# Optimization experiments

Hardware: AMD Instinct MI355X
Metric: run time of the kernel (lower is better)

The kernel has to match this reference:

```python
import jax, jax.numpy as jnp
import numpy as np

N_NODES = 500_000
D_IN = 256
D_ATT = 128
NUM_GRAPHS = 4096


def setup_inputs() -> dict:
    key = jax.random.key(0)
    k_x, k_b, k_w1, k_b1, k_w2, k_b2 = jax.random.split(key, 6)
    x = jax.random.normal(k_x, (N_NODES, D_IN), dtype=jnp.float32)
    batch = jnp.sort(jax.random.randint(k_b, (N_NODES,), 0, NUM_GRAPHS, dtype=jnp.int64))
    # attention_net params: Linear(D_IN, D_ATT) -> tanh -> Linear(D_ATT, 1)
    s1 = 1.0 / np.sqrt(D_IN)
    s2 = 1.0 / np.sqrt(D_ATT)
    W1 = jax.random.uniform(k_w1, (D_IN, D_ATT), minval=-s1, maxval=s1, dtype=jnp.float32)
    b1 = jax.random.uniform(k_b1, (D_ATT,), minval=-s1, maxval=s1, dtype=jnp.float32)
    W2 = jax.random.uniform(k_w2, (D_ATT, 1), minval=-s2, maxval=s2, dtype=jnp.float32)
    b2 = jax.random.uniform(k_b2, (1,), minval=-s2, maxval=s2, dtype=jnp.float32)
    return {"x": x, "batch": batch, "num_graphs": NUM_GRAPHS,
            "W1": W1, "b1": b1, "W2": W2, "b2": b2}


def reference(x, batch, num_graphs, W1, b1, W2, b2):
    # attention_weights = Linear -> tanh -> Linear  (dropout is identity in eval)
    h = jnp.tanh(x @ W1 + b1)              # [N, D_ATT]
    attn = h @ W2 + b2                      # [N, 1]
    weighted_x = x * attn                   # [N, D_IN]
    # global_add_pool: segment-sum over graph ids
    return jax.ops.segment_sum(weighted_x, batch, num_segments=num_graphs)  # [B, D_IN]
```

## Files before the change

### kernel.cpp

```cpp
#include <hip/hip_runtime.h>
#include <hip/hip_bf16.h>

#define NN     500000
#define DIN    256
#define DATT   128
#define NG     4096
#define MT     32
#define NT32   15625
#define NBLOCKS 768
#define TPB    21

typedef __attribute__((ext_vector_type(8))) short short8;
typedef __attribute__((ext_vector_type(4))) float f32x4;

__device__ __forceinline__ unsigned int pack2bf(float a, float b) {
    unsigned int ua = __float_as_uint(a) + 0x8000u;
    unsigned int ub = __float_as_uint(b) + 0x8000u;
    return __builtin_amdgcn_perm(ub, ua, 0x07060302);
}

__device__ __forceinline__ float tanh_fast(float v) {
    float e = __expf(2.f * v);
    return 1.f - 2.f * __builtin_amdgcn_rcpf(e + 1.f);
}

__device__ __forceinline__ void lds_barrier() {
    asm volatile("s_waitcnt lgkmcnt(0)" ::: "memory");
    __builtin_amdgcn_s_barrier();
    asm volatile("" ::: "memory");
}

__global__ void prep_w1t(const float* __restrict__ W1, unsigned short* __restrict__ W1t) {
    int c = blockIdx.x;
    int k = threadIdx.x;
    unsigned int u = __float_as_uint(W1[k * DATT + c]) + 0x8000u;
    W1t[c * DIN + k] = (unsigned short)(u >> 16);
}

__global__ __launch_bounds__(256, 3)
void attnpool_kernel(const float* __restrict__ x,
                     const int* __restrict__ batch,
                     const unsigned short* __restrict__ W1t,
                     const float* __restrict__ b1,
                     const float* __restrict__ W2,
                     const float* __restrict__ b2,
                     float* __restrict__ out)
{
    __shared__ unsigned short xb[2][MT * DIN];
    __shared__ float part[4][MT];

    const int t0 = blockIdx.x * TPB;
    if (t0 >= NT32) return;
    const int tEnd = (t0 + TPB < NT32) ? t0 + TPB : NT32;

    const int tid = threadIdx.x;
    const int w   = tid >> 6;
    const int l   = tid & 63;
    const int lr  = l & 15;
    const int lg  = l >> 4;

    short8 afr[16];
    {
        const unsigned short* A0 = W1t + (32 * w + lr) * DIN;
        #pragma unroll
        for (int kc = 0; kc < 8; ++kc) {
            afr[kc]     = *reinterpret_cast<const short8*>(A0 + 32 * kc + 8 * lg);
            afr[8 + kc] = *reinterpret_cast<const short8*>(A0 + 16 * DIN + 32 * kc + 8 * lg);
        }
    }
    float4 b1v[2], w2v[2];
    #pragma unroll
    for (int r2 = 0; r2 < 2; ++r2) {
        int c0 = 32 * w + 16 * r2 + 4 * lg;
        b1v[r2] = *reinterpret_cast<const float4*>(&b1[c0]);
        w2v[r2] = *reinterpret_cast<const float4*>(&W2[c0]);
    }
    const float b2s = b2[0];

    const float4* xg = (const float4*)x;
    float4 pf[8];
    {
        int base = t0 * (MT * 64);
        #pragma unroll
        for (int i = 0; i < 8; ++i) pf[i] = xg[base + tid + i * 256];
    }

    float accum = 0.f;
    int gcur = -1;
    int cur = 0;

    for (int t = t0; t < tEnd; ++t) {
        unsigned short* X = xb[cur];
        #pragma unroll
        for (int i = 0; i < 8; ++i) {
            int j = tid + i * 256;
            int r = j >> 6, c4 = j & 63;
            int byte = r * 512 + ((c4 * 8) ^ ((r & 7) << 4));
            *reinterpret_cast<uint2*>(reinterpret_cast<char*>(X) + byte) =
                make_uint2(pack2bf(pf[i].x, pf[i].y), pack2bf(pf[i].z, pf[i].w));
        }
        int bvt = -1;
        if (l < 32) {
            int g = batch[t * MT + l];
            bvt = ((unsigned)g < NG) ? g : -1;
        }
        lds_barrier();

        if (t + 1 < tEnd) {
            int base = (t + 1) * (MT * 64);
            #pragma unroll
            for (int i = 0; i < 8; ++i) pf[i] = xg[base + tid + i * 256];
        }

        f32x4 acc[2][2];
        #pragma unroll
        for (int r2 = 0; r2 < 2; ++r2)
            #pragma unroll
            for (int ct = 0; ct < 2; ++ct)
                acc[r2][ct] = (f32x4){0.f, 0.f, 0.f, 0.f};

        #pragma unroll
        for (int kc = 0; kc < 8; ++kc) {
            int ko = 32 * kc + 8 * lg;
            short8 bfr[2];
            #pragma unroll
            for (int ct = 0; ct < 2; ++ct) {
                int row = 16 * ct + lr;
                int byte = row * 512 + ((ko * 2) ^ ((row & 7) << 4));
                bfr[ct] = *reinterpret_cast<const short8*>(reinterpret_cast<const char*>(X) + byte);
            }
            #pragma unroll
            for (int ct = 0; ct < 2; ++ct) {
                acc[0][ct] = __builtin_amdgcn_mfma_f32_16x16x32_bf16(afr[kc],     bfr[ct], acc[0][ct], 0, 0, 0);
                acc[1][ct] = __builtin_amdgcn_mfma_f32_16x16x32_bf16(afr[8 + kc], bfr[ct], acc[1][ct], 0, 0, 0);
            }
        }

        #pragma unroll
        for (int ct = 0; ct < 2; ++ct) {
            float p = 0.f;
            #pragma unroll
            for (int r2 = 0; r2 < 2; ++r2) {
                p += tanh_fast(acc[r2][ct][0] + b1v[r2].x) * w2v[r2].x;
                p += tanh_fast(acc[r2][ct][1] + b1v[r2].y) * w2v[r2].y;
                p += tanh_fast(acc[r2][ct][2] + b1v[r2].z) * w2v[r2].z;
                p += tanh_fast(acc[r2][ct][3] + b1v[r2].w) * w2v[r2].w;
            }
            p += __shfl_xor(p, 16, 64);
            p += __shfl_xor(p, 32, 64);
            if (lg == 0) part[w][16 * ct + lr] = p;
        }
        lds_barrier();

        const int nd = l & 31;
        float va = b2s + part[0][nd] + part[1][nd] + part[2][nd] + part[3][nd];

        #pragma unroll
        for (int n = 0; n < MT; ++n) {
            int   g = __builtin_amdgcn_readlane(bvt, n);
            float a = __int_as_float(__builtin_amdgcn_readlane(__float_as_int(va), n));
            if (g != gcur) {
                if (gcur >= 0) atomicAdd(&out[gcur * DIN + tid], accum);
                accum = 0.f;
                gcur = g;
            }
            int byte = n * 512 + ((tid * 2) ^ ((n & 7) << 4));
            float xv = __uint_as_float(
                (unsigned int)(*reinterpret_cast<const unsigned short*>(
                    reinterpret_cast<const char*>(X) + byte)) << 16);
            accum = fmaf(a, xv, accum);
        }
        cur ^= 1;
    }
    if (gcur >= 0) atomicAdd(&out[gcur * DIN + tid], accum);
}

extern "C" void kernel_launch(void* const* d_in, const int* in_sizes, int n_in,
                              void* d_out, int out_size, void* d_ws, size_t ws_size,
                              hipStream_t stream) {
    const float* x     = (const float*)d_in[0];
    const int*   batch = (const int*)d_in[1];
    const float* W1 = (const float*)d_in[3];
    const float* b1 = (const float*)d_in[4];
    const float* W2 = (const float*)d_in[5];
    const float* b2 = (const float*)d_in[6];
    float* out = (float*)d_out;
    unsigned short* W1t = (unsigned short*)d_ws;

    hipMemsetAsync(out, 0, (size_t)NG * DIN * sizeof(float), stream);
    prep_w1t<<<DATT, DIN, 0, stream>>>(W1, W1t);
    attnpool_kernel<<<NBLOCKS, 256, 0, stream>>>(x, batch, W1t, b1, W2, b2, out);
}
```

Baseline: 156.7 us.

## Double block size to 512 threads, splitting MFMA columns and pooling across waves

Moves to 512-thread blocks with 8 waves. Each wave now computes 16 of the attention columns instead of 32, and the pooling loop is split so each half of the block handles 16 of the 32 nodes per tile. The grid shrinks from 768 to 512 blocks, each covering more tiles. The goal is to cut per-wave register pressure and serial pooling work and to raise occupancy. The cost is more LDS partial sums, more barrier participants and more atomics, since both halves flush separately.

```diff
diff --git a/kernel.cpp b/kernel.cpp
--- a/kernel.cpp
+++ b/kernel.cpp
@@ -7,8 +7,8 @@
 #define NG     4096
 #define MT     32
 #define NT32   15625
-#define NBLOCKS 768
-#define TPB    21
+#define NBLOCKS 512
+#define TPB    31
 
 typedef __attribute__((ext_vector_type(8))) short short8;
 typedef __attribute__((ext_vector_type(4))) float f32x4;
@@ -37,7 +37,7 @@
     W1t[c * DIN + k] = (unsigned short)(u >> 16);
 }
 
-__global__ __launch_bounds__(256, 3)
+__global__ __launch_bounds__(512, 4)
 void attnpool_kernel(const float* __restrict__ x,
                      const int* __restrict__ batch,
                      const unsigned short* __restrict__ W1t,
@@ -47,7 +47,7 @@
                      float* __restrict__ out)
 {
     __shared__ unsigned short xb[2][MT * DIN];
-    __shared__ float part[4][MT];
+    __shared__ float part[8][MT];
 
     const int t0 = blockIdx.x * TPB;
     if (t0 >= NT32) return;
@@ -59,41 +59,40 @@
     const int lr  = l & 15;
     const int lg  = l >> 4;
 
-    short8 afr[16];
+    short8 afr[8];
     {
-        const unsigned short* A0 = W1t + (32 * w + lr) * DIN;
+        const unsigned short* A0 = W1t + (16 * w + lr) * DIN;
         #pragma unroll
-        for (int kc = 0; kc < 8; ++kc) {
-            afr[kc]     = *reinterpret_cast<const short8*>(A0 + 32 * kc + 8 * lg);
-            afr[8 + kc] = *reinterpret_cast<const short8*>(A0 + 16 * DIN + 32 * kc + 8 * lg);
-        }
+        for (int kc = 0; kc < 8; ++kc)
+            afr[kc] = *reinterpret_cast<const short8*>(A0 + 32 * kc + 8 * lg);
     }
-    float4 b1v[2], w2v[2];
-    #pragma unroll
-    for (int r2 = 0; r2 < 2; ++r2) {
-        int c0 = 32 * w + 16 * r2 + 4 * lg;
-        b1v[r2] = *reinterpret_cast<const float4*>(&b1[c0]);
-        w2v[r2] = *reinterpret_cast<const float4*>(&W2[c0]);
+    float4 b1v, w2v;
+    {
+        int c0 = 16 * w + 4 * lg;
+        b1v = *reinterpret_cast<const float4*>(&b1[c0]);
+        w2v = *reinterpret_cast<const float4*>(&W2[c0]);
     }
     const float b2s = b2[0];
 
     const float4* xg = (const float4*)x;
-    float4 pf[8];
+    float4 pf[4];
     {
         int base = t0 * (MT * 64);
         #pragma unroll
-        for (int i = 0; i < 8; ++i) pf[i] = xg[base + tid + i * 256];
+        for (int i = 0; i < 4; ++i) pf[i] = xg[base + tid + i * 512];
     }
 
     float accum = 0.f;
     int gcur = -1;
     int cur = 0;
+    const int half = tid >> 8;
+    const int d    = tid & 255;
 
     for (int t = t0; t < tEnd; ++t) {
         unsigned short* X = xb[cur];
         #pragma unroll
-        for (int i = 0; i < 8; ++i) {
-            int j = tid + i * 256;
+        for (int i = 0; i < 4; ++i) {
+            int j = tid + i * 512;
             int r = j >> 6, c4 = j & 63;
             int byte = r * 512 + ((c4 * 8) ^ ((r & 7) << 4));
             *reinterpret_cast<uint2*>(reinterpret_cast<char*>(X) + byte) =
@@ -109,15 +108,12 @@
         if (t + 1 < tEnd) {
             int base = (t + 1) * (MT * 64);
             #pragma unroll
-            for (int i = 0; i < 8; ++i) pf[i] = xg[base + tid + i * 256];
+            for (int i = 0; i < 4; ++i) pf[i] = xg[base + tid + i * 512];
         }
 
-        f32x4 acc[2][2];
-        #pragma unroll
-        for (int r2 = 0; r2 < 2; ++r2)
-            #pragma unroll
-            for (int ct = 0; ct < 2; ++ct)
-                acc[r2][ct] = (f32x4){0.f, 0.f, 0.f, 0.f};
+        f32x4 acc[2];
+        acc[0] = (f32x4){0.f, 0.f, 0.f, 0.f};
+        acc[1] = (f32x4){0.f, 0.f, 0.f, 0.f};
 
         #pragma unroll
         for (int kc = 0; kc < 8; ++kc) {
@@ -129,23 +125,16 @@
                 int byte = row * 512 + ((ko * 2) ^ ((row & 7) << 4));
                 bfr[ct] = *reinterpret_cast<const short8*>(reinterpret_cast<const char*>(X) + byte);
             }
-            #pragma unroll
-            for (int ct = 0; ct < 2; ++ct) {
-                acc[0][ct] = __builtin_amdgcn_mfma_f32_16x16x32_bf16(afr[kc],     bfr[ct], acc[0][ct], 0, 0, 0);
-                acc[1][ct] = __builtin_amdgcn_mfma_f32_16x16x32_bf16(afr[8 + kc], bfr[ct], acc[1][ct], 0, 0, 0);
-            }
+            acc[0] = __builtin_amdgcn_mfma_f32_16x16x32_bf16(afr[kc], bfr[0], acc[0], 0, 0, 0);
+            acc[1] = __builtin_amdgcn_mfma_f32_16x16x32_bf16(afr[kc], bfr[1], acc[1], 0, 0, 0);
         }
 
         #pragma unroll
         for (int ct = 0; ct < 2; ++ct) {
-            float p = 0.f;
-            #pragma unroll
-            for (int r2 = 0; r2 < 2; ++r2) {
-                p += tanh_fast(acc[r2][ct][0] + b1v[r2].x) * w2v[r2].x;
-                p += tanh_fast(acc[r2][ct][1] + b1v[r2].y) * w2v[r2].y;
-                p += tanh_fast(acc[r2][ct][2] + b1v[r2].z) * w2v[r2].z;
-                p += tanh_fast(acc[r2][ct][3] + b1v[r2].w) * w2v[r2].w;
-            }
+            float p = tanh_fast(acc[ct][0] + b1v.x) * w2v.x
+                    + tanh_fast(acc[ct][1] + b1v.y) * w2v.y
+                    + tanh_fast(acc[ct][2] + b1v.z) * w2v.z
+                    + tanh_fast(acc[ct][3] + b1v.w) * w2v.w;
             p += __shfl_xor(p, 16, 64);
             p += __shfl_xor(p, 32, 64);
             if (lg == 0) part[w][16 * ct + lr] = p;
@@ -153,18 +142,20 @@
         lds_barrier();
 
         const int nd = l & 31;
-        float va = b2s + part[0][nd] + part[1][nd] + part[2][nd] + part[3][nd];
+        float va = b2s + part[0][nd] + part[1][nd] + part[2][nd] + part[3][nd]
+                       + part[4][nd] + part[5][nd] + part[6][nd] + part[7][nd];
 
         #pragma unroll
-        for (int n = 0; n < MT; ++n) {
-            int   g = __builtin_amdgcn_readlane(bvt, n);
-            float a = __int_as_float(__builtin_amdgcn_readlane(__float_as_int(va), n));
+        for (int n = 0; n < 16; ++n) {
+            int node = 16 * half + n;
+            int   g = __builtin_amdgcn_readlane(bvt, node);
+            float a = __int_as_float(__builtin_amdgcn_readlane(__float_as_int(va), node));
             if (g != gcur) {
-                if (gcur >= 0) atomicAdd(&out[gcur * DIN + tid], accum);
+                if (gcur >= 0) atomicAdd(&out[gcur * DIN + d], accum);
                 accum = 0.f;
                 gcur = g;
             }
-            int byte = n * 512 + ((tid * 2) ^ ((n & 7) << 4));
+            int byte = node * 512 + ((d * 2) ^ ((node & 7) << 4));
             float xv = __uint_as_float(
                 (unsigned int)(*reinterpret_cast<const unsigned short*>(
                     reinterpret_cast<const char*>(X) + byte)) << 16);
@@ -172,7 +163,7 @@
         }
         cur ^= 1;
     }
-    if (gcur >= 0) atomicAdd(&out[gcur * DIN + tid], accum);
+    if (gcur >= 0) atomicAdd(&out[gcur * DIN + d], accum);
 }
 
 extern "C" void kernel_launch(void* const* d_in, const int* in_sizes, int n_in,
@@ -189,5 +180,5 @@
 
     hipMemsetAsync(out, 0, (size_t)NG * DIN * sizeof(float), stream);
     prep_w1t<<<DATT, DIN, 0, stream>>>(W1, W1t);
-    attnpool_kernel<<<NBLOCKS, 256, 0, stream>>>(x, batch, W1t, b1, W2, b2, out);
+    attnpool_kernel<<<NBLOCKS, 512, 0, stream>>>(x, batch, W1t, b1, W2, b2, out);
 }
```

After: 136.6 us. 12.8% less time.
